# Performance work log

Hardware: AMD Instinct MI355X
Metric: run time of the kernel (lower is better)

## Reference

```python
import jax, jax.numpy as jnp
import numpy as np

R = 16
N = 524288          # hash table size per level
F = 2               # features per entry
MIN_RES, MAX_RES = 16, 2048
PRIME = 2654435761  # spatial hash prime (as in the torch module)
H = R * F           # MLP width = 32
M = 1048576         # number of query points

# resolutions exactly as in NGP.__init__
RESOLUTIONS = np.round(
    np.logspace(np.log2(MIN_RES), np.log2(MAX_RES), R, base=2)
).astype(np.float32)


def setup_inputs() -> dict:
    key = jax.random.key(0)
    ks = jax.random.split(key, 8)
    coords = jax.random.uniform(ks[0], (M, 2), dtype=jnp.float32)
    hash_features = jax.random.normal(ks[1], (R, N, F), dtype=jnp.float32)
    s = 1.0 / np.sqrt(H)
    W0 = jax.random.uniform(ks[2], (H, H), dtype=jnp.float32, minval=-s, maxval=s)
    b0 = jax.random.uniform(ks[3], (H,), dtype=jnp.float32, minval=-s, maxval=s)
    W1 = jax.random.uniform(ks[4], (H, H), dtype=jnp.float32, minval=-s, maxval=s)
    b1 = jax.random.uniform(ks[5], (H,), dtype=jnp.float32, minval=-s, maxval=s)
    W2 = jax.random.uniform(ks[6], (H, 3), dtype=jnp.float32, minval=-s, maxval=s)
    b2 = jax.random.uniform(ks[7], (3,), dtype=jnp.float32, minval=-s, maxval=s)
    return {"coords": coords, "hash_features": hash_features,
            "W0": W0, "b0": b0, "W1": W1, "b1": b1, "W2": W2, "b2": b2}


def _bilerp_hash(coords, hash_features):
    """coords [M,2] in [0,1); hash_features [R,N,F] -> [M, R*F]."""
    res = jnp.asarray(RESOLUTIONS)  # [R]
    prime = jnp.uint32(PRIME)
    n = jnp.uint32(N)

    def level(res_r, table_r):  # table_r: [N,F]
        x = coords * res_r                    # [M,2]
        xf = jnp.floor(x)
        w = x - xf                            # bilinear weights [M,2]
        xi = xf.astype(jnp.uint32)
        x0, y0 = xi[:, 0], xi[:, 1]

        def look(xx, yy):
            idx = (xx ^ (prime * yy)) % n     # spatial hash
            return table_r[idx]               # gather [M,F]

        wx, wy = w[:, :1], w[:, 1:]
        return (look(x0, y0) * (1 - wx) * (1 - wy)
                + look(x0, y0 + 1) * (1 - wx) * wy
                + look(x0 + 1, y0) * wx * (1 - wy)
                + look(x0 + 1, y0 + 1) * wx * wy)  # [M,F]

    feats = jax.vmap(level)(res, hash_features)   # [R,M,F]
    return jnp.transpose(feats, (1, 0, 2)).reshape(coords.shape[0], -1)  # [M,R*F]


def reference(coords, hash_features, W0, b0, W1, b1, W2, b2):
    f = _bilerp_hash(coords, hash_features)          # [M, 32]
    h = jax.nn.leaky_relu(f @ W0 + b0, 0.01)
    h = jax.nn.leaky_relu(h @ W1 + b1, 0.01)
    return h @ W2 + b2                               # [M, 3]
```

## Files before the change

kernel.cpp:

```cpp
#include <hip/hip_runtime.h>
#include <cmath>

#define R_LEVELS 16
#define N_TAB    524288u
#define N_MASK   (N_TAB - 1u)
#define PRIME_H  2654435761u
#define M_PTS    1048576
#define BDIM     128
#define NBUCK    (BDIM * BDIM)
#define NB4      (NBUCK / 4)
#define SBLK     256
#define STHR     1024
#define SPB      (M_PTS / SBLK)
#define SITER    (SPB / STHR)
#define NSEG     32
#define WSEG     (SBLK / NSEG)
#define XSTRIDE  36
#define NFRAG    384

typedef __attribute__((ext_vector_type(8)))  short bf16x8;
typedef __attribute__((ext_vector_type(16))) float f32x16;

union FragU { bf16x8 v; uint4 q; unsigned u[4]; uint2 u2[2]; unsigned short s[8]; };

struct ResArr { float r[R_LEVELS]; };

__device__ __forceinline__ unsigned pack_hi(float f0, float f1) {
    return __builtin_amdgcn_perm(__float_as_uint(f1), __float_as_uint(f0), 0x07060302u);
}
__device__ __forceinline__ unsigned pack_lo(float f0, float f1) {
    const float l0 = f0 - __uint_as_float(__float_as_uint(f0) & 0xffff0000u);
    const float l1 = f1 - __uint_as_float(__float_as_uint(f1) & 0xffff0000u);
    unsigned r;
    asm("v_cvt_pk_bf16_f32 %0, %1, %2" : "=v"(r) : "v"(l0), "v"(l1));
    return r;
}

__device__ __forceinline__ unsigned bucket_of(float x, float y) {
    unsigned bx = (unsigned)(x * (float)BDIM); if (bx >= BDIM) bx = BDIM - 1;
    unsigned by = (unsigned)(y * (float)BDIM); if (by >= BDIM) by = BDIM - 1;
    unsigned m = 0;
    #pragma unroll
    for (int i = 0; i < 7; ++i)
        m |= (((bx >> i) & 1u) << (2 * i)) | (((by >> i) & 1u) << (2 * i + 1));
    return m;
}

__global__ __launch_bounds__(STHR) void hist_k(const float2* __restrict__ coords,
                                               unsigned* __restrict__ C32,
                                               const float* __restrict__ W0,
                                               const float* __restrict__ W1,
                                               const float* __restrict__ W2,
                                               const float* __restrict__ b2,
                                               uint4* __restrict__ wbuf,
                                               float* __restrict__ b2p) {
    __shared__ unsigned h[NB4];
    const int t = threadIdx.x;
    const int w = blockIdx.x;
    #pragma unroll
    for (int i = t; i < NB4; i += STHR) h[i] = 0u;
    __syncthreads();
    #pragma unroll
    for (int k = 0; k < SITER; ++k) {
        const int p = w * SPB + k * STHR + t;
        const float2 c = coords[p];
        const unsigned b = bucket_of(c.x, c.y);
        atomicAdd(&h[b >> 2], 1u << ((b & 3u) * 8u));
    }
    __syncthreads();
    #pragma unroll
    for (int i = t; i < NB4; i += STHR)
        C32[(size_t)w * NB4 + i] = h[i];

    if (w == 0 && t < NFRAG) {
        const int fid  = t >> 6;
        const int lane = t & 63;
        const int l    = fid >> 1;
        const int kc   = fid & 1;
        const int l31  = lane & 31;
        const int hh   = lane >> 5;
        const float* Ws[3] = {W0, W1, W2};
        const int ncols[3] = {32, 32, 3};
        FragU H, L;
        #pragma unroll
        for (int e = 0; e < 8; ++e) {
            const int k = kc*16 + (e>>2)*8 + hh*4 + (e&3);
            const float wv = (l31 < ncols[l]) ? Ws[l][k*ncols[l] + l31] : 0.f;
            const unsigned short hi = (unsigned short)(__float_as_uint(wv) >> 16);
            const float rem = wv - __uint_as_float((unsigned)hi << 16);
            const unsigned u = __float_as_uint(rem);
            const unsigned short lo = (unsigned short)((u + 0x7fffu + ((u >> 16) & 1u)) >> 16);
            H.s[e] = hi;
            L.s[e] = lo;
        }
        wbuf[fid*64 + lane]         = H.q;
        wbuf[NFRAG + fid*64 + lane] = L.q;
        if (t < 32) b2p[t] = (t < 3) ? b2[t] : 0.f;
    }
}

__global__ __launch_bounds__(256) void scanw1_k(unsigned* __restrict__ C32,
                                                unsigned* __restrict__ P) {
    const int g = blockIdx.x * 256 + threadIdx.x;
    const int seg = g >> 12;
    const int b4  = g & (NB4 - 1);
    unsigned s0 = 0, s1 = 0, s2 = 0, s3 = 0;
    #pragma unroll
    for (int k = 0; k < WSEG; ++k) {
        const int w = seg * WSEG + k;
        const size_t i = (size_t)w * NB4 + b4;
        const unsigned u = C32[i];
        C32[i] = s0 | (s1 << 8) | (s2 << 16) | (s3 << 24);
        s0 += u & 255u;
        s1 += (u >> 8) & 255u;
        s2 += (u >> 16) & 255u;
        s3 += (u >> 24) & 255u;
    }
    const size_t pb = (size_t)seg * NBUCK + 4 * b4;
    P[pb + 0] = s0; P[pb + 1] = s1; P[pb + 2] = s2; P[pb + 3] = s3;
}

__global__ __launch_bounds__(256) void scanw2_k(unsigned* __restrict__ P,
                                                unsigned* __restrict__ T) {
    const int b = blockIdx.x * 256 + threadIdx.x;
    unsigned s = 0;
    #pragma unroll
    for (int seg = 0; seg < NSEG; ++seg) {
        const size_t i = (size_t)seg * NBUCK + b;
        const unsigned v = P[i];
        P[i] = s;
        s += v;
    }
    T[b] = s;
}

__global__ __launch_bounds__(256) void scan_k(const unsigned* __restrict__ T,
                                              unsigned* __restrict__ B) {
    __shared__ unsigned part[256];
    const int t = threadIdx.x;
    unsigned sum = 0;
    for (int k = 0; k < 64; ++k) sum += T[t * 64 + k];
    part[t] = sum;
    __syncthreads();
    for (int off = 1; off < 256; off <<= 1) {
        const unsigned v = (t >= off) ? part[t - off] : 0u;
        __syncthreads();
        part[t] += v;
        __syncthreads();
    }
    unsigned run = (t > 0) ? part[t - 1] : 0u;
    for (int k = 0; k < 64; ++k) {
        B[t * 64 + k] = run;
        run += T[t * 64 + k];
    }
}

__global__ __launch_bounds__(STHR) void scatter_k(const float2* __restrict__ coords,
                                                  const unsigned* __restrict__ C32,
                                                  const unsigned* __restrict__ P,
                                                  const unsigned* __restrict__ B,
                                                  float2* __restrict__ sxy,
                                                  unsigned* __restrict__ sidx) {
    __shared__ unsigned off[NBUCK];
    const int t = threadIdx.x;
    const int w = blockIdx.x;
    const int seg = w / WSEG;
    #pragma unroll
    for (int i4 = t; i4 < NB4; i4 += STHR) {
        const unsigned wrd = C32[(size_t)w * NB4 + i4];
        #pragma unroll
        for (int j = 0; j < 4; ++j) {
            const int b = 4 * i4 + j;
            off[b] = B[b] + P[(size_t)seg * NBUCK + b] + ((wrd >> (8 * j)) & 255u);
        }
    }
    __syncthreads();
    #pragma unroll
    for (int k = 0; k < SITER; ++k) {
        const int p = w * SPB + k * STHR + t;
        const float2 c = coords[p];
        const unsigned b = bucket_of(c.x, c.y);
        const unsigned pos = atomicAdd(&off[b], 1u);
        sxy[pos] = c;
        sidx[pos] = (unsigned)p;
    }
}

__global__ __launch_bounds__(256, 4) void ngp_mfma(
    const float2* __restrict__ pts,
    const unsigned* __restrict__ sidx,
    const float* __restrict__ hashf,
    const uint4* __restrict__ wbuf,
    const float* __restrict__ b0,
    const float* __restrict__ b1,
    const float* __restrict__ b2p,
    float* __restrict__ out, ResArr res)
{
    __shared__ unsigned short X[256 * XSTRIDE];

    const unsigned nwg = gridDim.x;
    const unsigned chunk = nwg >> 3;
    const unsigned sb = (blockIdx.x & 7u) * chunk + (blockIdx.x >> 3);
    const int tid = threadIdx.x;
    const int p = (int)(sb * 256u) + tid;

    const float2 c = pts[p];

    float f[32];
    float2 vA[16], vB[16];
    float2 wA[4], wB[4];

    auto issue = [&](int ck, float2* vv, float2* ww) {
        #pragma unroll
        for (int j = 0; j < 4; ++j) {
            const int r = ck * 4 + j;
            const float rr = res.r[r];
            const float x = c.x * rr;
            const float y = c.y * rr;
            const float xf = floorf(x);
            const float yf = floorf(y);
            ww[j].x = x - xf;
            ww[j].y = y - yf;
            const unsigned x0 = (unsigned)xf;
            const unsigned y0 = (unsigned)yf;
            const unsigned hy0 = PRIME_H * y0;
            const unsigned hy1 = PRIME_H * (y0 + 1u);
            const float2* tab = (const float2*)hashf + ((size_t)r << 19);
            vv[4*j+0] = tab[(x0 ^ hy0) & N_MASK];
            vv[4*j+1] = tab[(x0 ^ hy1) & N_MASK];
            vv[4*j+2] = tab[((x0 + 1u) ^ hy0) & N_MASK];
            vv[4*j+3] = tab[((x0 + 1u) ^ hy1) & N_MASK];
        }
    };
    auto consume = [&](int ck, const float2* vv, const float2* ww) {
        #pragma unroll
        for (int j = 0; j < 4; ++j) {
            const int r = ck * 4 + j;
            const float wx = ww[j].x, wy = ww[j].y;
            const float w00 = (1.f - wx) * (1.f - wy);
            const float w01 = (1.f - wx) * wy;
            const float w10 = wx * (1.f - wy);
            const float w11 = wx * wy;
            f[2*r+0] = vv[4*j+0].x*w00 + vv[4*j+1].x*w01 + vv[4*j+2].x*w10 + vv[4*j+3].x*w11;
            f[2*r+1] = vv[4*j+0].y*w00 + vv[4*j+1].y*w01 + vv[4*j+2].y*w10 + vv[4*j+3].y*w11;
        }
    };

    issue(0, vA, wA);
    issue(1, vB, wB);
    consume(0, vA, wA);
    issue(2, vA, wA);
    consume(1, vB, wB);
    issue(3, vB, wB);
    consume(2, vA, wA);
    consume(3, vB, wB);

    const int lane = tid & 63;
    const int wv   = tid >> 6;
    const int l31  = lane & 31;
    const int h    = lane >> 5;
    const int tb0  = wv * 64;
    const int tb1  = wv * 64 + 32;
    const int rowo = tid * XSTRIDE;

    auto ldx = [&](int ptl, int kc) -> FragU {
        FragU r;
        const int off = ptl * XSTRIDE + kc * 16 + h * 4;
        r.u2[0] = *(const uint2*)&X[off];
        r.u2[1] = *(const uint2*)&X[off + 8];
        return r;
    };

    #pragma unroll
    for (int q = 0; q < 8; ++q) {
        uint2 ph;
        ph.x = pack_hi(f[4*q+0], f[4*q+1]);
        ph.y = pack_hi(f[4*q+2], f[4*q+3]);
        *(uint2*)&X[rowo + 4*q] = ph;
    }
    FragU Ah0 = ldx(tb0 + l31, 0);
    FragU Ah1 = ldx(tb0 + l31, 1);
    FragU Bh0 = ldx(tb1 + l31, 0);
    FragU Bh1 = ldx(tb1 + l31, 1);

    #pragma unroll
    for (int q = 0; q < 8; ++q) {
        uint2 pl;
        pl.x = pack_lo(f[4*q+0], f[4*q+1]);
        pl.y = pack_lo(f[4*q+2], f[4*q+3]);
        *(uint2*)&X[rowo + 4*q] = pl;
    }
    FragU Al0 = ldx(tb0 + l31, 0);
    FragU Al1 = ldx(tb0 + l31, 1);
    FragU Bl0 = ldx(tb1 + l31, 0);
    FragU Bl1 = ldx(tb1 + l31, 1);

    auto bias_init = [&](const float* b) -> f32x16 {
        f32x16 a;
        #pragma unroll
        for (int q = 0; q < 4; ++q) {
            const float4 t = *(const float4*)(b + 8*q + 4*h);
            a[4*q+0] = t.x; a[4*q+1] = t.y; a[4*q+2] = t.z; a[4*q+3] = t.w;
        }
        return a;
    };

    f32x16 a0, a1;

    auto layer = [&](int l, const float* b) {
        FragU wh0, wl0, wh1, wl1;
        wh0.q = wbuf[(l*2+0)*64 + lane];
        wl0.q = wbuf[NFRAG + (l*2+0)*64 + lane];
        wh1.q = wbuf[(l*2+1)*64 + lane];
        wl1.q = wbuf[NFRAG + (l*2+1)*64 + lane];
        f32x16 A0 = bias_init(b);
        f32x16 A1 = A0;
        A0 = __builtin_amdgcn_mfma_f32_32x32x16_bf16(wh0.v, Ah0.v, A0, 0, 0, 0);
        A0 = __builtin_amdgcn_mfma_f32_32x32x16_bf16(wh0.v, Al0.v, A0, 0, 0, 0);
        A0 = __builtin_amdgcn_mfma_f32_32x32x16_bf16(wl0.v, Ah0.v, A0, 0, 0, 0);
        A0 = __builtin_amdgcn_mfma_f32_32x32x16_bf16(wh1.v, Ah1.v, A0, 0, 0, 0);
        A0 = __builtin_amdgcn_mfma_f32_32x32x16_bf16(wh1.v, Al1.v, A0, 0, 0, 0);
        A0 = __builtin_amdgcn_mfma_f32_32x32x16_bf16(wl1.v, Ah1.v, A0, 0, 0, 0);
        A1 = __builtin_amdgcn_mfma_f32_32x32x16_bf16(wh0.v, Bh0.v, A1, 0, 0, 0);
        A1 = __builtin_amdgcn_mfma_f32_32x32x16_bf16(wh0.v, Bl0.v, A1, 0, 0, 0);
        A1 = __builtin_amdgcn_mfma_f32_32x32x16_bf16(wl0.v, Bh0.v, A1, 0, 0, 0);
        A1 = __builtin_amdgcn_mfma_f32_32x32x16_bf16(wh1.v, Bh1.v, A1, 0, 0, 0);
        A1 = __builtin_amdgcn_mfma_f32_32x32x16_bf16(wh1.v, Bl1.v, A1, 0, 0, 0);
        A1 = __builtin_amdgcn_mfma_f32_32x32x16_bf16(wl1.v, Bh1.v, A1, 0, 0, 0);
        a0 = A0; a1 = A1;
    };

    auto act_repack = [&](const f32x16& a, FragU& xh0, FragU& xl0, FragU& xh1, FragU& xl1) {
        float v[16];
        #pragma unroll
        for (int r = 0; r < 16; ++r) v[r] = fmaxf(a[r], 0.01f * a[r]);
        #pragma unroll
        for (int w = 0; w < 4; ++w) {
            xh0.u[w] = pack_hi(v[2*w],   v[2*w+1]);
            xl0.u[w] = pack_lo(v[2*w],   v[2*w+1]);
            xh1.u[w] = pack_hi(v[8+2*w], v[8+2*w+1]);
            xl1.u[w] = pack_lo(v[8+2*w], v[8+2*w+1]);
        }
    };

    layer(0, b0);
    act_repack(a0, Ah0, Al0, Ah1, Al1);
    act_repack(a1, Bh0, Bl0, Bh1, Bl1);
    layer(1, b1);
    act_repack(a0, Ah0, Al0, Ah1, Al1);
    act_repack(a1, Bh0, Bl0, Bh1, Bl1);
    layer(2, b2p);

    if (h == 0) {
        const int pl0 = (int)(sb * 256u) + tb0 + l31;
        const int pl1 = (int)(sb * 256u) + tb1 + l31;
        const unsigned o0 = sidx ? sidx[pl0] : (unsigned)pl0;
        const unsigned o1 = sidx ? sidx[pl1] : (unsigned)pl1;
        out[(size_t)o0*3 + 0] = a0[0];
        out[(size_t)o0*3 + 1] = a0[1];
        out[(size_t)o0*3 + 2] = a0[2];
        out[(size_t)o1*3 + 0] = a1[0];
        out[(size_t)o1*3 + 1] = a1[1];
        out[(size_t)o1*3 + 2] = a1[2];
    }
}

extern "C" void kernel_launch(void* const* d_in, const int* in_sizes, int n_in,
                              void* d_out, int out_size, void* d_ws, size_t ws_size,
                              hipStream_t stream) {
    ResArr res;
    for (int i = 0; i < R_LEVELS; ++i)
        res.r[i] = (float)nearbyint(exp2(4.0 + (7.0 / 15.0) * (double)i));
    res.r[0] = 16.f;
    res.r[R_LEVELS - 1] = 2048.f;

    const float2* coords = (const float2*)d_in[0];
    const float* hashf   = (const float*)d_in[1];
    const float* W0      = (const float*)d_in[2];
    const float* b0      = (const float*)d_in[3];
    const float* W1      = (const float*)d_in[4];
    const float* b1      = (const float*)d_in[5];
    const float* W2      = (const float*)d_in[6];
    const float* b2      = (const float*)d_in[7];
    float* out           = (float*)d_out;

    const size_t off_C    = 0;
    const size_t off_P    = off_C + (size_t)SBLK * NB4 * 4;
    const size_t off_T    = off_P + (size_t)NSEG * NBUCK * 4;
    const size_t off_B    = off_T + NBUCK * 4;
    const size_t off_sxy  = off_B + NBUCK * 4;
    const size_t off_sidx = off_sxy + (size_t)M_PTS * sizeof(float2);
    const size_t off_wbuf = off_sidx + (size_t)M_PTS * 4;
    const size_t off_b2p  = off_wbuf + 2 * NFRAG * sizeof(uint4);
    const size_t need     = off_b2p + 32 * sizeof(float);

    dim3 blockM(256);
    dim3 gridM(M_PTS / 256);

    if (ws_size >= need) {
        unsigned* C32  = (unsigned*)((char*)d_ws + off_C);
        unsigned* P    = (unsigned*)((char*)d_ws + off_P);
        unsigned* T    = (unsigned*)((char*)d_ws + off_T);
        unsigned* B    = (unsigned*)((char*)d_ws + off_B);
        float2*   sxy  = (float2*)((char*)d_ws + off_sxy);
        unsigned* sidx = (unsigned*)((char*)d_ws + off_sidx);
        uint4*    wbuf = (uint4*)((char*)d_ws + off_wbuf);
        float*    b2p  = (float*)((char*)d_ws + off_b2p);

        hipLaunchKernelGGL(hist_k,    dim3(SBLK), dim3(STHR), 0, stream,
                           coords, C32, W0, W1, W2, b2, wbuf, b2p);
        hipLaunchKernelGGL(scanw1_k,  dim3(NSEG * NB4 / 256), dim3(256), 0, stream, C32, P);
        hipLaunchKernelGGL(scanw2_k,  dim3(NBUCK / 256), dim3(256), 0, stream, P, T);
        hipLaunchKernelGGL(scan_k,    dim3(1), dim3(256), 0, stream, T, B);
        hipLaunchKernelGGL(scatter_k, dim3(SBLK), dim3(STHR), 0, stream, coords, C32, P, B, sxy, sidx);
        hipLaunchKernelGGL(ngp_mfma,  gridM, blockM, 0, stream,
                           sxy, sidx, hashf, wbuf, b0, b1, b2p, out, res);
    }
}
```

Before: 121.2 us.

## Replace per-block histogram scans with global atomic histogram and atomic scatter

```diff
diff --git a/kernel.cpp b/kernel.cpp
--- a/kernel.cpp
+++ b/kernel.cpp
@@ -13,8 +13,6 @@
 #define STHR     1024
 #define SPB      (M_PTS / SBLK)
 #define SITER    (SPB / STHR)
-#define NSEG     32
-#define WSEG     (SBLK / NSEG)
 #define XSTRIDE  36
 #define NFRAG    384
 
@@ -47,7 +45,7 @@
 }
 
 __global__ __launch_bounds__(STHR) void hist_k(const float2* __restrict__ coords,
-                                               unsigned* __restrict__ C32,
+                                               unsigned* __restrict__ T,
                                                const float* __restrict__ W0,
                                                const float* __restrict__ W1,
                                                const float* __restrict__ W2,
@@ -69,8 +67,16 @@
     }
     __syncthreads();
     #pragma unroll
-    for (int i = t; i < NB4; i += STHR)
-        C32[(size_t)w * NB4 + i] = h[i];
+    for (int i4 = t; i4 < NB4; i4 += STHR) {
+        const unsigned wrd = h[i4];
+        if (wrd) {
+            #pragma unroll
+            for (int j = 0; j < 4; ++j) {
+                const unsigned cnt = (wrd >> (8 * j)) & 255u;
+                if (cnt) atomicAdd(&T[4 * i4 + j], cnt);
+            }
+        }
+    }
 
     if (w == 0 && t < NFRAG) {
         const int fid  = t >> 6;
@@ -99,88 +105,44 @@
     }
 }
 
-__global__ __launch_bounds__(256) void scanw1_k(unsigned* __restrict__ C32,
-                                                unsigned* __restrict__ P) {
-    const int g = blockIdx.x * 256 + threadIdx.x;
-    const int seg = g >> 12;
-    const int b4  = g & (NB4 - 1);
-    unsigned s0 = 0, s1 = 0, s2 = 0, s3 = 0;
-    #pragma unroll
-    for (int k = 0; k < WSEG; ++k) {
-        const int w = seg * WSEG + k;
-        const size_t i = (size_t)w * NB4 + b4;
-        const unsigned u = C32[i];
-        C32[i] = s0 | (s1 << 8) | (s2 << 16) | (s3 << 24);
-        s0 += u & 255u;
-        s1 += (u >> 8) & 255u;
-        s2 += (u >> 16) & 255u;
-        s3 += (u >> 24) & 255u;
-    }
-    const size_t pb = (size_t)seg * NBUCK + 4 * b4;
-    P[pb + 0] = s0; P[pb + 1] = s1; P[pb + 2] = s2; P[pb + 3] = s3;
-}
-
-__global__ __launch_bounds__(256) void scanw2_k(unsigned* __restrict__ P,
-                                                unsigned* __restrict__ T) {
-    const int b = blockIdx.x * 256 + threadIdx.x;
-    unsigned s = 0;
-    #pragma unroll
-    for (int seg = 0; seg < NSEG; ++seg) {
-        const size_t i = (size_t)seg * NBUCK + b;
-        const unsigned v = P[i];
-        P[i] = s;
-        s += v;
-    }
-    T[b] = s;
-}
-
-__global__ __launch_bounds__(256) void scan_k(const unsigned* __restrict__ T,
-                                              unsigned* __restrict__ B) {
-    __shared__ unsigned part[256];
+__global__ __launch_bounds__(1024) void scan_k(const unsigned* __restrict__ T,
+                                               unsigned* __restrict__ B) {
+    __shared__ unsigned part[1024];
     const int t = threadIdx.x;
+    unsigned loc[16];
     unsigned sum = 0;
-    for (int k = 0; k < 64; ++k) sum += T[t * 64 + k];
+    #pragma unroll
+    for (int k = 0; k < 16; ++k) {
+        const unsigned v = T[t * 16 + k];
+        loc[k] = sum;
+        sum += v;
+    }
     part[t] = sum;
     __syncthreads();
-    for (int off = 1; off < 256; off <<= 1) {
+    for (int off = 1; off < 1024; off <<= 1) {
         const unsigned v = (t >= off) ? part[t - off] : 0u;
         __syncthreads();
         part[t] += v;
         __syncthreads();
     }
-    unsigned run = (t > 0) ? part[t - 1] : 0u;
-    for (int k = 0; k < 64; ++k) {
-        B[t * 64 + k] = run;
-        run += T[t * 64 + k];
-    }
+    const unsigned base = (t > 0) ? part[t - 1] : 0u;
+    #pragma unroll
+    for (int k = 0; k < 16; ++k)
+        B[t * 16 + k] = base + loc[k];
 }
 
 __global__ __launch_bounds__(STHR) void scatter_k(const float2* __restrict__ coords,
-                                                  const unsigned* __restrict__ C32,
-                                                  const unsigned* __restrict__ P,
-                                                  const unsigned* __restrict__ B,
+                                                  unsigned* __restrict__ B,
                                                   float2* __restrict__ sxy,
                                                   unsigned* __restrict__ sidx) {
-    __shared__ unsigned off[NBUCK];
     const int t = threadIdx.x;
     const int w = blockIdx.x;
-    const int seg = w / WSEG;
-    #pragma unroll
-    for (int i4 = t; i4 < NB4; i4 += STHR) {
-        const unsigned wrd = C32[(size_t)w * NB4 + i4];
-        #pragma unroll
-        for (int j = 0; j < 4; ++j) {
-            const int b = 4 * i4 + j;
-            off[b] = B[b] + P[(size_t)seg * NBUCK + b] + ((wrd >> (8 * j)) & 255u);
-        }
-    }
-    __syncthreads();
     #pragma unroll
     for (int k = 0; k < SITER; ++k) {
         const int p = w * SPB + k * STHR + t;
         const float2 c = coords[p];
         const unsigned b = bucket_of(c.x, c.y);
-        const unsigned pos = atomicAdd(&off[b], 1u);
+        const unsigned pos = atomicAdd(&B[b], 1u);
         sxy[pos] = c;
         sidx[pos] = (unsigned)p;
     }
@@ -354,8 +316,8 @@
     if (h == 0) {
         const int pl0 = (int)(sb * 256u) + tb0 + l31;
         const int pl1 = (int)(sb * 256u) + tb1 + l31;
-        const unsigned o0 = sidx ? sidx[pl0] : (unsigned)pl0;
-        const unsigned o1 = sidx ? sidx[pl1] : (unsigned)pl1;
+        const unsigned o0 = sidx[pl0];
+        const unsigned o1 = sidx[pl1];
         out[(size_t)o0*3 + 0] = a0[0];
         out[(size_t)o0*3 + 1] = a0[1];
         out[(size_t)o0*3 + 2] = a0[2];
@@ -384,9 +346,7 @@
     const float* b2      = (const float*)d_in[7];
     float* out           = (float*)d_out;
 
-    const size_t off_C    = 0;
-    const size_t off_P    = off_C + (size_t)SBLK * NB4 * 4;
-    const size_t off_T    = off_P + (size_t)NSEG * NBUCK * 4;
+    const size_t off_T    = 0;
     const size_t off_B    = off_T + NBUCK * 4;
     const size_t off_sxy  = off_B + NBUCK * 4;
     const size_t off_sidx = off_sxy + (size_t)M_PTS * sizeof(float2);
@@ -398,8 +358,6 @@
     dim3 gridM(M_PTS / 256);
 
     if (ws_size >= need) {
-        unsigned* C32  = (unsigned*)((char*)d_ws + off_C);
-        unsigned* P    = (unsigned*)((char*)d_ws + off_P);
         unsigned* T    = (unsigned*)((char*)d_ws + off_T);
         unsigned* B    = (unsigned*)((char*)d_ws + off_B);
         float2*   sxy  = (float2*)((char*)d_ws + off_sxy);
@@ -407,12 +365,12 @@
         uint4*    wbuf = (uint4*)((char*)d_ws + off_wbuf);
         float*    b2p  = (float*)((char*)d_ws + off_b2p);
 
+        hipMemsetAsync(T, 0, NBUCK * 4, stream);
         hipLaunchKernelGGL(hist_k,    dim3(SBLK), dim3(STHR), 0, stream,
-                           coords, C32, W0, W1, W2, b2, wbuf, b2p);
-        hipLaunchKernelGGL(scanw1_k,  dim3(NSEG * NB4 / 256), dim3(256), 0, stream, C32, P);
-        hipLaunchKernelGGL(scanw2_k,  dim3(NBUCK / 256), dim3(256), 0, stream, P, T);
-        hipLaunchKernelGGL(scan_k,    dim3(1), dim3(256), 0, stream, T, B);
-        hipLaunchKernelGGL(scatter_k, dim3(SBLK), dim3(STHR), 0, stream, coords, C32, P, B, sxy, sidx);
+                           coords, T, W0, W1, W2, b2, wbuf, b2p);
+        hipLaunchKernelGGL(scan_k,    dim3(1), dim3(1024), 0, stream, T, B);
+        hipLaunchKernelGGL(scatter_k, dim3(SBLK), dim3(STHR), 0, stream,
+                           coords, B, sxy, sidx);
         hipLaunchKernelGGL(ngp_mfma,  gridM, blockM, 0, stream,
                            sxy, sidx, hashf, wbuf, b0, b1, b2p, out, res);
     }
```

Result: slower. 196.5 us (+62.1%).
